# Kernel optimization log

Measured on AMD Instinct MI355X. Metric: run time of the kernel, lower is better.

The kernel has to match this reference:

```python
import jax, jax.numpy as jnp
import numpy as np

LN_EPS = 1e-5

def _ln(x):
    # haiku LayerNorm([-1], create_scale=False, create_offset=False)
    mu = x.mean(axis=-1, keepdims=True)
    var = x.var(axis=-1, keepdims=True)
    return (x - mu) * jax.lax.rsqrt(var + LN_EPS)

def setup_inputs() -> dict:
    key = jax.random.key(0)
    ks = jax.random.split(key, 10)
    N, L, P = 512, 256, 64
    inp = {
        "local": jax.random.normal(ks[0], (N, L), jnp.float32),
        "pair": jax.random.normal(ks[1], (N, N, P), jnp.float32),
        "mask": jax.random.randint(ks[2], (N,), 0, 2, jnp.int32),
        "W_pair_gate": jax.random.normal(ks[3], (P, 2 * P), jnp.float32) / np.sqrt(P),
        "W_pair_value": jax.random.normal(ks[4], (P, 2 * P), jnp.float32) / np.sqrt(P),
        "W_left_gate": jax.random.normal(ks[5], (L, 2 * P), jnp.float32) / np.sqrt(L),
        "W_left_value": jax.random.normal(ks[6], (L, 2 * P), jnp.float32) / np.sqrt(L),
        "W_right_gate": jax.random.normal(ks[7], (L, 2 * P), jnp.float32) / np.sqrt(L),
        "W_right_value": jax.random.normal(ks[8], (L, 2 * P), jnp.float32) / np.sqrt(L),
        "W_out": jax.random.normal(ks[9], (3 * P, P), jnp.float32) / np.sqrt(3 * P),
    }
    return inp

def reference(local, pair, mask, W_pair_gate, W_pair_value, W_left_gate,
              W_left_value, W_right_gate, W_right_value, W_out):
    maskb = mask.astype(bool)
    pair_mask = maskb[:, None] & maskb[None, :]                  # (N, N)
    l = _ln(local)                                               # (N, L)
    p = _ln(pair)                                                # (N, N, P)
    pair_gate = p @ W_pair_gate                                  # (N, N, 2P)
    pair_value = p @ W_pair_value                                # (N, N, 2P)
    # left: broadcast local over axis 0/1, gelu-gate, mask, reduce over j
    left_gate = jax.nn.gelu((l @ W_left_gate)[:, None] + pair_gate)
    left_value = (l @ W_left_value)[None, :] + pair_value
    left = jnp.where(pair_mask[..., None], left_gate * left_value, 0).sum(axis=1)  # (N, 2P)
    right_gate = jax.nn.gelu((l @ W_right_gate)[None, :] + pair_gate)
    right_value = (l @ W_right_value)[:, None] + pair_value
    right = jnp.where(pair_mask[..., None], right_gate * right_value, 0).sum(axis=0)  # (N, 2P)
    paired_pseudo_local = _ln(left[:, None] + right[None, :])    # (N, N, 2P)
    pair_hidden = jnp.concatenate((p, paired_pseudo_local), axis=-1)  # (N, N, 3P)
    return pair_hidden @ W_out                                   # (N, N, P)
```

## Files before the change

### kernel.cpp

```cpp
#include <hip/hip_runtime.h>
#include <math.h>

#define LN_EPS 1e-5f


typedef __bf16 bf16x8 __attribute__((ext_vector_type(8)));
typedef float f32x16 __attribute__((ext_vector_type(16)));

__device__ __forceinline__ float gelu_f(float x) {
    float x2 = x * x;
    float e = __builtin_amdgcn_exp2f(x * fmaf(0.10294423f, x2, 2.3022079f));
    float r = __builtin_amdgcn_rcpf(e + 1.0f);
    return fmaf(-x, r, x);
}

__global__ void kM(const int* __restrict__ mask, int* __restrict__ act) {
    const int t = threadIdx.x;
    const int lane = t & 63, w = t >> 6;
    __shared__ int wcnt_sh[8];
    int m = (mask[t] != 0);
    unsigned long long b = __ballot(m);
    if (lane == 0) wcnt_sh[w] = __popcll(b);
    __syncthreads();
    int base = 0;
    for (int u = 0; u < w; ++u) base += wcnt_sh[u];
    int pos = base + __popcll(b & ((1ull << lane) - 1ull));
    if (m) act[1 + pos] = t;
    if (t == 511) act[0] = base + __popcll(b);
}

__global__ __launch_bounds__(256) void kA(
    const float* __restrict__ loc,
    const float* __restrict__ Wlg, const float* __restrict__ Wlv,
    const float* __restrict__ Wrg, const float* __restrict__ Wrv,
    float* __restrict__ proj) {
    __shared__ float ln_sh[8][260];
    __shared__ float red_sh[128][9];
    const int t = threadIdx.x;
    const int i0 = blockIdx.x * 8;
    const int mat = blockIdx.y;
    const float* __restrict__ W = (mat == 0) ? Wlg : (mat == 1) ? Wlv
                                 : (mat == 2) ? Wrg : Wrv;
    {
        int row = t >> 5, l32 = t & 31;
        const float4* src = (const float4*)(loc + (i0 + row) * 256);
        float4 v0 = src[l32 * 2];
        float4 v1 = src[l32 * 2 + 1];
        float s = (v0.x + v0.y) + (v0.z + v0.w) + (v1.x + v1.y) + (v1.z + v1.w);
        float ss = v0.x * v0.x + v0.y * v0.y + v0.z * v0.z + v0.w * v0.w +
                   v1.x * v1.x + v1.y * v1.y + v1.z * v1.z + v1.w * v1.w;
#pragma unroll
        for (int off = 1; off < 32; off <<= 1) {
            s += __shfl_xor(s, off);
            ss += __shfl_xor(ss, off);
        }
        float mu = s * (1.f / 256.f);
        float rs = rsqrtf(ss * (1.f / 256.f) - mu * mu + LN_EPS);
        float4 o0, o1;
        o0.x = (v0.x - mu) * rs; o0.y = (v0.y - mu) * rs;
        o0.z = (v0.z - mu) * rs; o0.w = (v0.w - mu) * rs;
        o1.x = (v1.x - mu) * rs; o1.y = (v1.y - mu) * rs;
        o1.z = (v1.z - mu) * rs; o1.w = (v1.w - mu) * rs;
        *(float4*)&ln_sh[row][l32 * 8] = o0;
        *(float4*)&ln_sh[row][l32 * 8 + 4] = o1;
    }
    __syncthreads();

    const int n = t & 127;
    const int kh = t >> 7;
    float acc[8] = {0.f, 0.f, 0.f, 0.f, 0.f, 0.f, 0.f, 0.f};
#pragma unroll 2
    for (int c = 0; c < 32; ++c) {
        const int kc = kh * 128 + c * 4;
        float w0 = W[(kc + 0) * 128 + n];
        float w1 = W[(kc + 1) * 128 + n];
        float w2 = W[(kc + 2) * 128 + n];
        float w3 = W[(kc + 3) * 128 + n];
#pragma unroll
        for (int r = 0; r < 8; ++r) {
            float4 l4 = *(const float4*)&ln_sh[r][kc];
            acc[r] += l4.x * w0 + l4.y * w1 + l4.z * w2 + l4.w * w3;
        }
    }
    if (kh == 1) {
#pragma unroll
        for (int r = 0; r < 8; ++r) red_sh[n][r] = acc[r];
    }
    __syncthreads();
    if (kh == 0) {
#pragma unroll
        for (int r = 0; r < 8; ++r)
            proj[mat * 65536 + (i0 + r) * 128 + n] = acc[r] + red_sh[n][r];
    }
}

#define KB_TI 8
__global__ __launch_bounds__(256) void kB(
    const float* __restrict__ pair, const int* __restrict__ act,
    const float* __restrict__ Wg, const float* __restrict__ Wv,
    const float* __restrict__ lg, const float* __restrict__ lv,
    const float* __restrict__ rg, const float* __restrict__ rv,
    float* __restrict__ left, float* __restrict__ right) {
    __shared__ __bf16 A_sh[2][32][72];
    __shared__ float lv_sh[32][132];
    __shared__ float rg_sh[32][132];
    __shared__ int ji_sh[32];
    __shared__ int ii_sh[KB_TI];

    const int cnt = act[0];
    const int j0 = blockIdx.x * 32;
    const int ibase = blockIdx.y * KB_TI;
    if (j0 >= cnt || ibase >= cnt) return;
    const int nact = min(KB_TI, cnt - ibase);

    const int t = threadIdx.x;
    const int lane = t & 63;
    const int w = t >> 6;
    const int c = lane & 31;
    const int half = lane >> 5;
    const int n = w * 32 + c;

    if (t < 32) ji_sh[t] = act[1 + min(j0 + t, cnt - 1)];
    if (t >= 64 && t < 64 + KB_TI) ii_sh[t - 64] = act[1 + min(ibase + (t - 64), cnt - 1)];
    __syncthreads();

    bf16x8 bg[4], bv[4];
#pragma unroll
    for (int kt = 0; kt < 4; ++kt) {
        bf16x8 vg, vv;
#pragma unroll
        for (int e = 0; e < 8; ++e) {
            int kr = kt * 16 + half * 8 + e;
            vg[e] = (__bf16)Wg[kr * 128 + n];
            vv[e] = (__bf16)Wv[kr * 128 + n];
        }
        bg[kt] = vg; bv[kt] = vv;
    }

    for (int idx = t; idx < 32 * 128; idx += 256) {
        int jj = idx >> 7, nn = idx & 127;
        int j = ji_sh[jj];
        lv_sh[jj][nn] = lv[j * 128 + nn];
        rg_sh[jj][nn] = rg[j * 128 + nn];
    }

    const int srow = t >> 3;
    const int kseg = (t & 7) * 8;
    float4 p0, p1;
    float plg, prv;

    {
        int iF = act[1 + ibase];
        const float* src = pair + ((size_t)iF * 512 + ji_sh[srow]) * 64 + kseg;
        p0 = *(const float4*)src;
        p1 = *(const float4*)(src + 4);
        plg = lg[iF * 128 + n];
        prv = rv[iF * 128 + n];
    }

    auto lnwrite = [&](int buf) {
        float s = (p0.x + p0.y) + (p0.z + p0.w) + (p1.x + p1.y) + (p1.z + p1.w);
        float ss = p0.x * p0.x + p0.y * p0.y + p0.z * p0.z + p0.w * p0.w +
                   p1.x * p1.x + p1.y * p1.y + p1.z * p1.z + p1.w * p1.w;
        s += __shfl_xor(s, 1); ss += __shfl_xor(ss, 1);
        s += __shfl_xor(s, 2); ss += __shfl_xor(ss, 2);
        s += __shfl_xor(s, 4); ss += __shfl_xor(ss, 4);
        float mu = s * (1.f / 64.f);
        float rs = rsqrtf(ss * (1.f / 64.f) - mu * mu + LN_EPS);
        bf16x8 o;
        o[0] = (__bf16)((p0.x - mu) * rs); o[1] = (__bf16)((p0.y - mu) * rs);
        o[2] = (__bf16)((p0.z - mu) * rs); o[3] = (__bf16)((p0.w - mu) * rs);
        o[4] = (__bf16)((p1.x - mu) * rs); o[5] = (__bf16)((p1.y - mu) * rs);
        o[6] = (__bf16)((p1.z - mu) * rs); o[7] = (__bf16)((p1.w - mu) * rs);
        *(bf16x8*)&A_sh[buf][srow][kseg] = o;
    };
    lnwrite(0);
    __syncthreads();

    float racc[16];
#pragma unroll
    for (int r = 0; r < 16; ++r) racc[r] = 0.f;

    for (int ii = 0; ii < nact; ++ii) {
        const int i = ii_sh[ii];
        const float lgi = plg;
        const float rvi = prv;
        if (ii + 1 < nact) {
            int iF = ii_sh[ii + 1];
            const float* src = pair + ((size_t)iF * 512 + ji_sh[srow]) * 64 + kseg;
            p0 = *(const float4*)src;
            p1 = *(const float4*)(src + 4);
            plg = lg[iF * 128 + n];
            prv = rv[iF * 128 + n];
        }

        f32x16 ag = {}; f32x16 av = {};
#pragma unroll
        for (int kt = 0; kt < 4; ++kt) {
            bf16x8 af = *(const bf16x8*)&A_sh[ii & 1][c][kt * 16 + half * 8];
            ag = __builtin_amdgcn_mfma_f32_32x32x16_bf16(af, bg[kt], ag, 0, 0, 0);
            av = __builtin_amdgcn_mfma_f32_32x32x16_bf16(af, bv[kt], av, 0, 0, 0);
        }

        float lsum = 0.f;
#pragma unroll
        for (int r = 0; r < 16; ++r) {
            int m = 4 * half + (r & 3) + 8 * (r >> 2);
            float pg = ag[r], pv = av[r];
            float lres = gelu_f(lgi + pg) * (lv_sh[m][n] + pv);
            float rres = gelu_f(rg_sh[m][n] + pg) * (rvi + pv);
            if (j0 + m < cnt) lsum += lres;
            racc[r] += rres;
        }
        float tot = lsum + __shfl_xor(lsum, 32);
        if (lane < 32) atomicAdd(&left[i * 128 + n], tot);

        if (ii + 1 < nact) lnwrite((ii + 1) & 1);
        __syncthreads();
    }

#pragma unroll
    for (int r = 0; r < 16; ++r) {
        int m = 4 * half + (r & 3) + 8 * (r >> 2);
        if (j0 + m < cnt) atomicAdd(&right[ji_sh[m] * 128 + n], racc[r]);
    }
}

__global__ void kD1(const float* __restrict__ left, const float* __restrict__ right,
                    const float* __restrict__ W_out,
                    float* __restrict__ Aw, float* __restrict__ Bw,
                    float* __restrict__ sums, float* __restrict__ cs) {
    const int t = threadIdx.x;
    const int r = blockIdx.x;
    const int which = blockIdx.y;
    const float* src = which ? right : left;
    __shared__ float row_sh[128];
    __shared__ float red[4];
    float v = src[r * 128 + t];
    row_sh[t] = v;
    float s = v, ss = v * v;
#pragma unroll
    for (int off = 1; off < 64; off <<= 1) {
        s += __shfl_xor(s, off);
        ss += __shfl_xor(ss, off);
    }
    int wid = t >> 6, lane = t & 63;
    if (lane == 0) { red[wid * 2] = s; red[wid * 2 + 1] = ss; }
    __syncthreads();
    if (t == 0) {
        sums[which * 1024 + r] = red[0] + red[2];
        sums[which * 1024 + 512 + r] = red[1] + red[3];
    }
    if (t < 64) {
        float a = 0.f;
        const float* W2 = W_out + 64 * 64;
#pragma unroll 8
        for (int m = 0; m < 128; ++m) a += row_sh[m] * W2[m * 64 + t];
        (which ? Bw : Aw)[r * 64 + t] = a;
    }
    if (r == 0 && which == 0 && t < 64) {
        float c0 = 0.f, c1 = 0.f;
        for (int k = 0; k < 64; ++k) c0 += W_out[k * 64 + t];
        for (int m = 0; m < 128; ++m) c1 += W_out[(64 + m) * 64 + t];
        cs[t] = c0;
        cs[64 + t] = c1;
    }
}

__global__ void kD2(const float* __restrict__ left, const float* __restrict__ right,
                    float* __restrict__ C) {
    __shared__ float l_sh[32][68];
    __shared__ float r_sh[32][68];
    const int t = threadIdx.x;
    const int tx = t & 15, ty = t >> 4;
    const int i0 = blockIdx.x * 32, j0 = blockIdx.y * 32;
    float acc00 = 0.f, acc01 = 0.f, acc10 = 0.f, acc11 = 0.f;
    for (int kc = 0; kc < 128; kc += 64) {
        __syncthreads();
#pragma unroll
        for (int u = 0; u < 2; ++u) {
            int fi = t + u * 256;
            int row = fi >> 4, kq = (fi & 15) * 4;
            float4 lv4 = *(const float4*)(left + (i0 + row) * 128 + kc + kq);
            float4 rv4 = *(const float4*)(right + (j0 + row) * 128 + kc + kq);
            *(float4*)&l_sh[row][kq] = lv4;
            *(float4*)&r_sh[row][kq] = rv4;
        }
        __syncthreads();
#pragma unroll 8
        for (int k = 0; k < 64; ++k) {
            float l0 = l_sh[ty * 2 + 0][k], l1 = l_sh[ty * 2 + 1][k];
            float r0 = r_sh[tx * 2 + 0][k], r1 = r_sh[tx * 2 + 1][k];
            acc00 += l0 * r0; acc01 += l0 * r1;
            acc10 += l1 * r0; acc11 += l1 * r1;
        }
    }
    C[(size_t)(i0 + ty * 2 + 0) * 512 + j0 + tx * 2 + 0] = acc00;
    C[(size_t)(i0 + ty * 2 + 0) * 512 + j0 + tx * 2 + 1] = acc01;
    C[(size_t)(i0 + ty * 2 + 1) * 512 + j0 + tx * 2 + 0] = acc10;
    C[(size_t)(i0 + ty * 2 + 1) * 512 + j0 + tx * 2 + 1] = acc11;
}

__global__ __launch_bounds__(256) void kC(
    const float* __restrict__ pair, const float* __restrict__ Wout,
    const float* __restrict__ Aw, const float* __restrict__ Bw,
    const float* __restrict__ Cw, const float* __restrict__ sums,
    const float* __restrict__ cs, float* __restrict__ out) {
    __shared__ __bf16 A_sh[2][64][72];
    __shared__ float rs_sh[128], q_sh[128];

    const int t = threadIdx.x;
    const int lane = t & 63;
    const int w = t >> 6;
    const int c = lane & 31;
    const int half = lane >> 5;
    const int i0 = blockIdx.x * 2;
    const int j0 = blockIdx.y * 64;
    const int isub = w & 1;
    const int nt = w >> 1;
    const int n = nt * 32 + c;
    const int i = i0 + isub;

    bf16x8 bo[4];
#pragma unroll
    for (int kt = 0; kt < 4; ++kt) {
        bf16x8 v;
#pragma unroll
        for (int e = 0; e < 8; ++e)
            v[e] = (__bf16)Wout[(kt * 16 + half * 8 + e) * 64 + n];
        bo[kt] = v;
    }

    if (t < 128) {
        int ip = i0 + (t >> 6);
        int jp = j0 + (t & 63);
        float sumL = sums[ip], ssL = sums[512 + ip];
        float sR = sums[1024 + jp], ssR = sums[1536 + jp];
        float Cv = Cw[(size_t)ip * 512 + jp];
        float mu = (sumL + sR) * (1.f / 128.f);
        float var = (ssL + 2.f * Cv + ssR) * (1.f / 128.f) - mu * mu;
        float rs = rsqrtf(var + LN_EPS);
        rs_sh[t] = rs;
        q_sh[t] = rs * mu;
    }
    {
        int row = t >> 1;
        int kc = (t & 1) * 32;
        const float* src = pair + ((size_t)(i0 + (row >> 6)) * 512 + j0 + (row & 63)) * 64 + kc;
        float4 v[8];
#pragma unroll
        for (int u = 0; u < 8; ++u) v[u] = ((const float4*)src)[u];
        float s = 0.f, ss = 0.f;
#pragma unroll
        for (int u = 0; u < 8; ++u) {
            s += (v[u].x + v[u].y) + (v[u].z + v[u].w);
            ss += v[u].x * v[u].x + v[u].y * v[u].y + v[u].z * v[u].z + v[u].w * v[u].w;
        }
        s += __shfl_xor(s, 1); ss += __shfl_xor(ss, 1);
        float mu = s * (1.f / 64.f);
        float rs = rsqrtf(ss * (1.f / 64.f) - mu * mu + LN_EPS);
#pragma unroll
        for (int u = 0; u < 2; ++u) {
            bf16x8 o;
            o[0] = (__bf16)((v[u*2].x - mu) * rs);   o[1] = (__bf16)((v[u*2].y - mu) * rs);
            o[2] = (__bf16)((v[u*2].z - mu) * rs);   o[3] = (__bf16)((v[u*2].w - mu) * rs);
            o[4] = (__bf16)((v[u*2+1].x - mu) * rs); o[5] = (__bf16)((v[u*2+1].y - mu) * rs);
            o[6] = (__bf16)((v[u*2+1].z - mu) * rs); o[7] = (__bf16)((v[u*2+1].w - mu) * rs);
            *(bf16x8*)&A_sh[row >> 6][row & 63][kc + u * 8] = o;
        }
#pragma unroll
        for (int u = 2; u < 4; ++u) {
            bf16x8 o;
            o[0] = (__bf16)((v[u*2].x - mu) * rs);   o[1] = (__bf16)((v[u*2].y - mu) * rs);
            o[2] = (__bf16)((v[u*2].z - mu) * rs);   o[3] = (__bf16)((v[u*2].w - mu) * rs);
            o[4] = (__bf16)((v[u*2+1].x - mu) * rs); o[5] = (__bf16)((v[u*2+1].y - mu) * rs);
            o[6] = (__bf16)((v[u*2+1].z - mu) * rs); o[7] = (__bf16)((v[u*2+1].w - mu) * rs);
            *(bf16x8*)&A_sh[row >> 6][row & 63][kc + u * 8] = o;
        }
    }
    __syncthreads();

    f32x16 acc0 = {}; f32x16 acc1 = {};
#pragma unroll
    for (int kt = 0; kt < 4; ++kt) {
        bf16x8 a0 = *(const bf16x8*)&A_sh[isub][c][kt * 16 + half * 8];
        bf16x8 a1 = *(const bf16x8*)&A_sh[isub][32 + c][kt * 16 + half * 8];
        acc0 = __builtin_amdgcn_mfma_f32_32x32x16_bf16(a0, bo[kt], acc0, 0, 0, 0);
        acc1 = __builtin_amdgcn_mfma_f32_32x32x16_bf16(a1, bo[kt], acc1, 0, 0, 0);
    }

    const float A_in = Aw[i * 64 + n];
    const float cs1n = cs[64 + n];

#pragma unroll
    for (int mt = 0; mt < 2; ++mt) {
#pragma unroll
        for (int r = 0; r < 16; ++r) {
            int m = mt * 32 + 4 * half + (r & 3) + 8 * (r >> 2);
            float a = mt ? acc1[r] : acc0[r];
            float Bv = Bw[(j0 + m) * 64 + n];
            float rs = rs_sh[isub * 64 + m];
            float q = q_sh[isub * 64 + m];
            out[((size_t)i * 512 + j0 + m) * 64 + n] =
                fmaf(rs, A_in + Bv, fmaf(-q, cs1n, a));
        }
    }
}

extern "C" void kernel_launch(void* const* d_in, const int* in_sizes, int n_in,
                              void* d_out, int out_size, void* d_ws, size_t ws_size,
                              hipStream_t stream) {
    const float* loc  = (const float*)d_in[0];
    const float* pair = (const float*)d_in[1];
    const int*   mask = (const int*)d_in[2];
    const float* Wpg  = (const float*)d_in[3];
    const float* Wpv  = (const float*)d_in[4];
    const float* Wlg  = (const float*)d_in[5];
    const float* Wlv  = (const float*)d_in[6];
    const float* Wrg  = (const float*)d_in[7];
    const float* Wrv  = (const float*)d_in[8];
    const float* Wout = (const float*)d_in[9];
    float* out = (float*)d_out;
    float* ws = (float*)d_ws;

    float* proj  = ws;
    float* left  = ws + 262144;
    float* right = ws + 327680;
    float* Aw    = ws + 393216;
    float* Bw    = ws + 425984;
    float* Cw    = ws + 458752;
    float* sums  = ws + 720896;
    float* cs    = ws + 722944;
    int*   act   = (int*)(ws + 723072);

    hipMemsetAsync(left, 0, 2 * 65536 * sizeof(float), stream);

    kM<<<1, 512, 0, stream>>>(mask, act);
    kA<<<dim3(64, 4), 256, 0, stream>>>(loc, Wlg, Wlv, Wrg, Wrv, proj);
    kB<<<dim3(16, 64), 256, 0, stream>>>(pair, act, Wpg, Wpv,
                                         proj, proj + 65536, proj + 131072,
                                         proj + 196608, left, right);
    kD1<<<dim3(512, 2), 128, 0, stream>>>(left, right, Wout, Aw, Bw, sums, cs);
    kD2<<<dim3(16, 16), 256, 0, stream>>>(left, right, Cw);
    kC<<<dim3(256, 8), 256, 0, stream>>>(pair, Wout, Aw, Bw, Cw, sums, cs, out);
}
```

Baseline: 198.7 us.

## Fuse small kernels, drop memset, register-cache gathers, simplify output GEMM kernel

The mask compaction and the zeroing of the left/right buffers move into extra blocks of the projection kernel, which removes the memset and one launch. The two reduction kernels kD1/kD2 merge into one launch. kB keeps the gathered lv/rg values and a validity bitmask in registers instead of shared memory. kC now handles one row i per block and loads pair directly into MFMA operand registers, with no shared-memory staging and no barrier. It recomputes the per-(i,j) LayerNorm statistics inline in the epilogue, trading extra rsqrt work and repeated loads for fewer launches and less synchronisation.

```diff
diff --git a/kernel.cpp b/kernel.cpp
--- a/kernel.cpp
+++ b/kernel.cpp
@@ -14,29 +14,51 @@
     return fmaf(-x, r, x);
 }
 
-__global__ void kM(const int* __restrict__ mask, int* __restrict__ act) {
-    const int t = threadIdx.x;
-    const int lane = t & 63, w = t >> 6;
-    __shared__ int wcnt_sh[8];
-    int m = (mask[t] != 0);
-    unsigned long long b = __ballot(m);
-    if (lane == 0) wcnt_sh[w] = __popcll(b);
-    __syncthreads();
-    int base = 0;
-    for (int u = 0; u < w; ++u) base += wcnt_sh[u];
-    int pos = base + __popcll(b & ((1ull << lane) - 1ull));
-    if (m) act[1 + pos] = t;
-    if (t == 511) act[0] = base + __popcll(b);
-}
-
 __global__ __launch_bounds__(256) void kA(
     const float* __restrict__ loc,
     const float* __restrict__ Wlg, const float* __restrict__ Wlv,
     const float* __restrict__ Wrg, const float* __restrict__ Wrv,
-    float* __restrict__ proj) {
+    float* __restrict__ proj, const int* __restrict__ mask,
+    int* __restrict__ act, float* __restrict__ left, float* __restrict__ right) {
+    const int t = threadIdx.x;
+    if (blockIdx.x == 64) {
+        if (blockIdx.y == 1) {
+            float4 z = {0.f, 0.f, 0.f, 0.f};
+            for (int idx = t; idx < 16384; idx += 256) ((float4*)left)[idx] = z;
+        } else if (blockIdx.y == 2) {
+            float4 z = {0.f, 0.f, 0.f, 0.f};
+            for (int idx = t; idx < 16384; idx += 256) ((float4*)right)[idx] = z;
+        } else if (blockIdx.y == 0) {
+            __shared__ int cnt_sh[8];
+            const int lane = t & 63, wv = t >> 6;
+            int msave[2];
+            unsigned long long bsave[2];
+#pragma unroll
+            for (int ch = 0; ch < 2; ++ch) {
+                int m = (mask[ch * 256 + t] != 0);
+                unsigned long long b = __ballot(m);
+                if (lane == 0) cnt_sh[ch * 4 + wv] = __popcll(b);
+                msave[ch] = m;
+                bsave[ch] = b;
+            }
+            __syncthreads();
+#pragma unroll
+            for (int ch = 0; ch < 2; ++ch) {
+                int base = 0;
+                for (int u = 0; u < ch * 4 + wv; ++u) base += cnt_sh[u];
+                int pos = base + __popcll(bsave[ch] & ((1ull << lane) - 1ull));
+                if (msave[ch]) act[1 + pos] = ch * 256 + t;
+            }
+            if (t == 0) {
+                int ctot = 0;
+                for (int u = 0; u < 8; ++u) ctot += cnt_sh[u];
+                act[0] = ctot;
+            }
+        }
+        return;
+    }
     __shared__ float ln_sh[8][260];
     __shared__ float red_sh[128][9];
-    const int t = threadIdx.x;
     const int i0 = blockIdx.x * 8;
     const int mat = blockIdx.y;
     const float* __restrict__ W = (mat == 0) ? Wlg : (mat == 1) ? Wlv
@@ -102,8 +124,6 @@
     const float* __restrict__ rg, const float* __restrict__ rv,
     float* __restrict__ left, float* __restrict__ right) {
     __shared__ __bf16 A_sh[2][32][72];
-    __shared__ float lv_sh[32][132];
-    __shared__ float rg_sh[32][132];
     __shared__ int ji_sh[32];
     __shared__ int ii_sh[KB_TI];
 
@@ -137,20 +157,23 @@
         bg[kt] = vg; bv[kt] = vv;
     }
 
-    for (int idx = t; idx < 32 * 128; idx += 256) {
-        int jj = idx >> 7, nn = idx & 127;
-        int j = ji_sh[jj];
-        lv_sh[jj][nn] = lv[j * 128 + nn];
-        rg_sh[jj][nn] = rg[j * 128 + nn];
+    float lvr[16], rgr[16];
+    unsigned jmask = 0;
+#pragma unroll
+    for (int r = 0; r < 16; ++r) {
+        int m = 4 * half + (r & 3) + 8 * (r >> 2);
+        int j = ji_sh[m];
+        lvr[r] = lv[j * 128 + n];
+        rgr[r] = rg[j * 128 + n];
+        if (j0 + m < cnt) jmask |= (1u << r);
     }
 
     const int srow = t >> 3;
     const int kseg = (t & 7) * 8;
     float4 p0, p1;
     float plg, prv;
-
     {
-        int iF = act[1 + ibase];
+        int iF = ii_sh[0];
         const float* src = pair + ((size_t)iF * 512 + ji_sh[srow]) * 64 + kseg;
         p0 = *(const float4*)src;
         p1 = *(const float4*)(src + 4);
@@ -205,11 +228,10 @@
         float lsum = 0.f;
 #pragma unroll
         for (int r = 0; r < 16; ++r) {
-            int m = 4 * half + (r & 3) + 8 * (r >> 2);
             float pg = ag[r], pv = av[r];
-            float lres = gelu_f(lgi + pg) * (lv_sh[m][n] + pv);
-            float rres = gelu_f(rg_sh[m][n] + pg) * (rvi + pv);
-            if (j0 + m < cnt) lsum += lres;
+            float lres = gelu_f(lgi + pg) * (lvr[r] + pv);
+            float rres = gelu_f(rgr[r] + pg) * (rvi + pv);
+            lsum += ((jmask >> r) & 1) ? lres : 0.f;
             racc[r] += rres;
         }
         float tot = lsum + __shfl_xor(lsum, 32);
@@ -221,84 +243,89 @@
 
 #pragma unroll
     for (int r = 0; r < 16; ++r) {
-        int m = 4 * half + (r & 3) + 8 * (r >> 2);
-        if (j0 + m < cnt) atomicAdd(&right[ji_sh[m] * 128 + n], racc[r]);
-    }
-}
-
-__global__ void kD1(const float* __restrict__ left, const float* __restrict__ right,
-                    const float* __restrict__ W_out,
-                    float* __restrict__ Aw, float* __restrict__ Bw,
-                    float* __restrict__ sums, float* __restrict__ cs) {
+        if ((jmask >> r) & 1) {
+            int m = 4 * half + (r & 3) + 8 * (r >> 2);
+            atomicAdd(&right[ji_sh[m] * 128 + n], racc[r]);
+        }
+    }
+}
+
+__global__ __launch_bounds__(256) void kD(
+    const float* __restrict__ left, const float* __restrict__ right,
+    const float* __restrict__ W_out,
+    float* __restrict__ Aw, float* __restrict__ Bw,
+    float* __restrict__ sums, float* __restrict__ cs, float* __restrict__ C) {
+    const int bx = blockIdx.x;
     const int t = threadIdx.x;
-    const int r = blockIdx.x;
-    const int which = blockIdx.y;
-    const float* src = which ? right : left;
-    __shared__ float row_sh[128];
-    __shared__ float red[4];
-    float v = src[r * 128 + t];
-    row_sh[t] = v;
-    float s = v, ss = v * v;
-#pragma unroll
-    for (int off = 1; off < 64; off <<= 1) {
-        s += __shfl_xor(s, off);
-        ss += __shfl_xor(ss, off);
-    }
-    int wid = t >> 6, lane = t & 63;
-    if (lane == 0) { red[wid * 2] = s; red[wid * 2 + 1] = ss; }
-    __syncthreads();
-    if (t == 0) {
-        sums[which * 1024 + r] = red[0] + red[2];
-        sums[which * 1024 + 512 + r] = red[1] + red[3];
-    }
-    if (t < 64) {
-        float a = 0.f;
-        const float* W2 = W_out + 64 * 64;
+    if (bx < 256) {
+        __shared__ float l_sh[32][68];
+        __shared__ float r_sh[32][68];
+        const int tx = t & 15, ty = t >> 4;
+        const int i0 = (bx & 15) * 32, j0 = (bx >> 4) * 32;
+        float acc00 = 0.f, acc01 = 0.f, acc10 = 0.f, acc11 = 0.f;
+        for (int kc = 0; kc < 128; kc += 64) {
+            __syncthreads();
+#pragma unroll
+            for (int u = 0; u < 2; ++u) {
+                int fi = t + u * 256;
+                int row = fi >> 4, kq = (fi & 15) * 4;
+                float4 lv4 = *(const float4*)(left + (i0 + row) * 128 + kc + kq);
+                float4 rv4 = *(const float4*)(right + (j0 + row) * 128 + kc + kq);
+                *(float4*)&l_sh[row][kq] = lv4;
+                *(float4*)&r_sh[row][kq] = rv4;
+            }
+            __syncthreads();
 #pragma unroll 8
-        for (int m = 0; m < 128; ++m) a += row_sh[m] * W2[m * 64 + t];
-        (which ? Bw : Aw)[r * 64 + t] = a;
-    }
-    if (r == 0 && which == 0 && t < 64) {
-        float c0 = 0.f, c1 = 0.f;
-        for (int k = 0; k < 64; ++k) c0 += W_out[k * 64 + t];
-        for (int m = 0; m < 128; ++m) c1 += W_out[(64 + m) * 64 + t];
-        cs[t] = c0;
-        cs[64 + t] = c1;
-    }
-}
-
-__global__ void kD2(const float* __restrict__ left, const float* __restrict__ right,
-                    float* __restrict__ C) {
-    __shared__ float l_sh[32][68];
-    __shared__ float r_sh[32][68];
-    const int t = threadIdx.x;
-    const int tx = t & 15, ty = t >> 4;
-    const int i0 = blockIdx.x * 32, j0 = blockIdx.y * 32;
-    float acc00 = 0.f, acc01 = 0.f, acc10 = 0.f, acc11 = 0.f;
-    for (int kc = 0; kc < 128; kc += 64) {
+            for (int k = 0; k < 64; ++k) {
+                float l0 = l_sh[ty * 2 + 0][k], l1 = l_sh[ty * 2 + 1][k];
+                float r0 = r_sh[tx * 2 + 0][k], r1 = r_sh[tx * 2 + 1][k];
+                acc00 += l0 * r0; acc01 += l0 * r1;
+                acc10 += l1 * r0; acc11 += l1 * r1;
+            }
+        }
+        C[(size_t)(i0 + ty * 2 + 0) * 512 + j0 + tx * 2 + 0] = acc00;
+        C[(size_t)(i0 + ty * 2 + 0) * 512 + j0 + tx * 2 + 1] = acc01;
+        C[(size_t)(i0 + ty * 2 + 1) * 512 + j0 + tx * 2 + 0] = acc10;
+        C[(size_t)(i0 + ty * 2 + 1) * 512 + j0 + tx * 2 + 1] = acc11;
+    } else {
+        const int id = bx - 256;
+        const int which = id >> 8;
+        const int sub = t >> 7;
+        const int tt = t & 127;
+        const int r = (id & 255) * 2 + sub;
+        const float* src = which ? right : left;
+        __shared__ float row_sh[2][128];
+        __shared__ float red[2][4];
+        float v = src[r * 128 + tt];
+        row_sh[sub][tt] = v;
+        float s = v, ss = v * v;
+#pragma unroll
+        for (int off = 1; off < 64; off <<= 1) {
+            s += __shfl_xor(s, off);
+            ss += __shfl_xor(ss, off);
+        }
+        int wid = tt >> 6, lane = tt & 63;
+        if (lane == 0) { red[sub][wid * 2] = s; red[sub][wid * 2 + 1] = ss; }
         __syncthreads();
-#pragma unroll
-        for (int u = 0; u < 2; ++u) {
-            int fi = t + u * 256;
-            int row = fi >> 4, kq = (fi & 15) * 4;
-            float4 lv4 = *(const float4*)(left + (i0 + row) * 128 + kc + kq);
-            float4 rv4 = *(const float4*)(right + (j0 + row) * 128 + kc + kq);
-            *(float4*)&l_sh[row][kq] = lv4;
-            *(float4*)&r_sh[row][kq] = rv4;
-        }
-        __syncthreads();
+        if (tt == 0) {
+            sums[which * 1024 + r] = red[sub][0] + red[sub][2];
+            sums[which * 1024 + 512 + r] = red[sub][1] + red[sub][3];
+        }
+        if (tt < 64) {
+            float a = 0.f;
+            const float* W2 = W_out + 64 * 64;
 #pragma unroll 8
-        for (int k = 0; k < 64; ++k) {
-            float l0 = l_sh[ty * 2 + 0][k], l1 = l_sh[ty * 2 + 1][k];
-            float r0 = r_sh[tx * 2 + 0][k], r1 = r_sh[tx * 2 + 1][k];
-            acc00 += l0 * r0; acc01 += l0 * r1;
-            acc10 += l1 * r0; acc11 += l1 * r1;
-        }
-    }
-    C[(size_t)(i0 + ty * 2 + 0) * 512 + j0 + tx * 2 + 0] = acc00;
-    C[(size_t)(i0 + ty * 2 + 0) * 512 + j0 + tx * 2 + 1] = acc01;
-    C[(size_t)(i0 + ty * 2 + 1) * 512 + j0 + tx * 2 + 0] = acc10;
-    C[(size_t)(i0 + ty * 2 + 1) * 512 + j0 + tx * 2 + 1] = acc11;
+            for (int m = 0; m < 128; ++m) a += row_sh[sub][m] * W2[m * 64 + tt];
+            (which ? Bw : Aw)[r * 64 + tt] = a;
+        }
+        if (id == 0 && t < 64) {
+            float c0 = 0.f, c1 = 0.f;
+            for (int k = 0; k < 64; ++k) c0 += W_out[k * 64 + t];
+            for (int m = 0; m < 128; ++m) c1 += W_out[(64 + m) * 64 + t];
+            cs[t] = c0;
+            cs[64 + t] = c1;
+        }
+    }
 }
 
 __global__ __launch_bounds__(256) void kC(
@@ -306,104 +333,74 @@
     const float* __restrict__ Aw, const float* __restrict__ Bw,
     const float* __restrict__ Cw, const float* __restrict__ sums,
     const float* __restrict__ cs, float* __restrict__ out) {
-    __shared__ __bf16 A_sh[2][64][72];
-    __shared__ float rs_sh[128], q_sh[128];
-
     const int t = threadIdx.x;
     const int lane = t & 63;
     const int w = t >> 6;
     const int c = lane & 31;
     const int half = lane >> 5;
-    const int i0 = blockIdx.x * 2;
+    const int i = blockIdx.x;
     const int j0 = blockIdx.y * 64;
-    const int isub = w & 1;
+    const int mt = w & 1;
     const int nt = w >> 1;
     const int n = nt * 32 + c;
-    const int i = i0 + isub;
-
+    const int jrow = j0 + mt * 32 + c;
+
+    const float* __restrict__ asrc = pair + ((size_t)i * 512 + jrow) * 64 + half * 8;
+    float4 v[8];
+#pragma unroll
+    for (int kt = 0; kt < 4; ++kt) {
+        v[2 * kt] = *(const float4*)(asrc + kt * 16);
+        v[2 * kt + 1] = *(const float4*)(asrc + kt * 16 + 4);
+    }
     bf16x8 bo[4];
 #pragma unroll
     for (int kt = 0; kt < 4; ++kt) {
-        bf16x8 v;
+        bf16x8 bb;
 #pragma unroll
         for (int e = 0; e < 8; ++e)
-            v[e] = (__bf16)Wout[(kt * 16 + half * 8 + e) * 64 + n];
-        bo[kt] = v;
-    }
-
-    if (t < 128) {
-        int ip = i0 + (t >> 6);
-        int jp = j0 + (t & 63);
-        float sumL = sums[ip], ssL = sums[512 + ip];
-        float sR = sums[1024 + jp], ssR = sums[1536 + jp];
-        float Cv = Cw[(size_t)ip * 512 + jp];
-        float mu = (sumL + sR) * (1.f / 128.f);
-        float var = (ssL + 2.f * Cv + ssR) * (1.f / 128.f) - mu * mu;
-        float rs = rsqrtf(var + LN_EPS);
-        rs_sh[t] = rs;
-        q_sh[t] = rs * mu;
-    }
-    {
-        int row = t >> 1;
-        int kc = (t & 1) * 32;
-        const float* src = pair + ((size_t)(i0 + (row >> 6)) * 512 + j0 + (row & 63)) * 64 + kc;
-        float4 v[8];
-#pragma unroll
-        for (int u = 0; u < 8; ++u) v[u] = ((const float4*)src)[u];
-        float s = 0.f, ss = 0.f;
-#pragma unroll
-        for (int u = 0; u < 8; ++u) {
-            s += (v[u].x + v[u].y) + (v[u].z + v[u].w);
-            ss += v[u].x * v[u].x + v[u].y * v[u].y + v[u].z * v[u].z + v[u].w * v[u].w;
-        }
-        s += __shfl_xor(s, 1); ss += __shfl_xor(ss, 1);
-        float mu = s * (1.f / 64.f);
-        float rs = rsqrtf(ss * (1.f / 64.f) - mu * mu + LN_EPS);
+            bb[e] = (__bf16)Wout[(kt * 16 + half * 8 + e) * 64 + n];
+        bo[kt] = bb;
+    }
+    float s = 0.f, ss = 0.f;
+#pragma unroll
+    for (int u = 0; u < 8; ++u) {
+        s += (v[u].x + v[u].y) + (v[u].z + v[u].w);
+        ss += v[u].x * v[u].x + v[u].y * v[u].y + v[u].z * v[u].z + v[u].w * v[u].w;
+    }
+    s += __shfl_xor(s, 32);
+    ss += __shfl_xor(ss, 32);
+    float mu = s * (1.f / 64.f);
+    float rs = rsqrtf(ss * (1.f / 64.f) - mu * mu + LN_EPS);
+
+    f32x16 acc = {};
+#pragma unroll
+    for (int kt = 0; kt < 4; ++kt) {
+        bf16x8 af;
 #pragma unroll
         for (int u = 0; u < 2; ++u) {
-            bf16x8 o;
-            o[0] = (__bf16)((v[u*2].x - mu) * rs);   o[1] = (__bf16)((v[u*2].y - mu) * rs);
-            o[2] = (__bf16)((v[u*2].z - mu) * rs);   o[3] = (__bf16)((v[u*2].w - mu) * rs);
-            o[4] = (__bf16)((v[u*2+1].x - mu) * rs); o[5] = (__bf16)((v[u*2+1].y - mu) * rs);
-            o[6] = (__bf16)((v[u*2+1].z - mu) * rs); o[7] = (__bf16)((v[u*2+1].w - mu) * rs);
-            *(bf16x8*)&A_sh[row >> 6][row & 63][kc + u * 8] = o;
-        }
-#pragma unroll
-        for (int u = 2; u < 4; ++u) {
-            bf16x8 o;
-            o[0] = (__bf16)((v[u*2].x - mu) * rs);   o[1] = (__bf16)((v[u*2].y - mu) * rs);
-            o[2] = (__bf16)((v[u*2].z - mu) * rs);   o[3] = (__bf16)((v[u*2].w - mu) * rs);
-            o[4] = (__bf16)((v[u*2+1].x - mu) * rs); o[5] = (__bf16)((v[u*2+1].y - mu) * rs);
-            o[6] = (__bf16)((v[u*2+1].z - mu) * rs); o[7] = (__bf16)((v[u*2+1].w - mu) * rs);
-            *(bf16x8*)&A_sh[row >> 6][row & 63][kc + u * 8] = o;
-        }
-    }
-    __syncthreads();
-
-    f32x16 acc0 = {}; f32x16 acc1 = {};
-#pragma unroll
-    for (int kt = 0; kt < 4; ++kt) {
-        bf16x8 a0 = *(const bf16x8*)&A_sh[isub][c][kt * 16 + half * 8];
-        bf16x8 a1 = *(const bf16x8*)&A_sh[isub][32 + c][kt * 16 + half * 8];
-        acc0 = __builtin_amdgcn_mfma_f32_32x32x16_bf16(a0, bo[kt], acc0, 0, 0, 0);
-        acc1 = __builtin_amdgcn_mfma_f32_32x32x16_bf16(a1, bo[kt], acc1, 0, 0, 0);
+            float4 vv = v[2 * kt + u];
+            af[u * 4 + 0] = (__bf16)((vv.x - mu) * rs);
+            af[u * 4 + 1] = (__bf16)((vv.y - mu) * rs);
+            af[u * 4 + 2] = (__bf16)((vv.z - mu) * rs);
+            af[u * 4 + 3] = (__bf16)((vv.w - mu) * rs);
+        }
+        acc = __builtin_amdgcn_mfma_f32_32x32x16_bf16(af, bo[kt], acc, 0, 0, 0);
     }
 
     const float A_in = Aw[i * 64 + n];
     const float cs1n = cs[64 + n];
-
-#pragma unroll
-    for (int mt = 0; mt < 2; ++mt) {
-#pragma unroll
-        for (int r = 0; r < 16; ++r) {
-            int m = mt * 32 + 4 * half + (r & 3) + 8 * (r >> 2);
-            float a = mt ? acc1[r] : acc0[r];
-            float Bv = Bw[(j0 + m) * 64 + n];
-            float rs = rs_sh[isub * 64 + m];
-            float q = q_sh[isub * 64 + m];
-            out[((size_t)i * 512 + j0 + m) * 64 + n] =
-                fmaf(rs, A_in + Bv, fmaf(-q, cs1n, a));
-        }
+    const float sumLi = sums[i], ssLi = sums[512 + i];
+#pragma unroll
+    for (int r = 0; r < 16; ++r) {
+        int jp = j0 + mt * 32 + 4 * half + (r & 3) + 8 * (r >> 2);
+        float sR = sums[1024 + jp], ssR = sums[1536 + jp];
+        float Cv = Cw[(size_t)i * 512 + jp];
+        float Bv = Bw[jp * 64 + n];
+        float mu_s = (sumLi + sR) * (1.f / 128.f);
+        float var_s = fmaf(-mu_s, mu_s, (ssLi + 2.f * Cv + ssR) * (1.f / 128.f));
+        float rs_s = rsqrtf(var_s + LN_EPS);
+        out[((size_t)i * 512 + jp) * 64 + n] =
+            fmaf(rs_s, (A_in + Bv) - mu_s * cs1n, acc[r]);
     }
 }
 
@@ -433,14 +430,11 @@
     float* cs    = ws + 722944;
     int*   act   = (int*)(ws + 723072);
 
-    hipMemsetAsync(left, 0, 2 * 65536 * sizeof(float), stream);
-
-    kM<<<1, 512, 0, stream>>>(mask, act);
-    kA<<<dim3(64, 4), 256, 0, stream>>>(loc, Wlg, Wlv, Wrg, Wrv, proj);
+    kA<<<dim3(65, 4), 256, 0, stream>>>(loc, Wlg, Wlv, Wrg, Wrv, proj,
+                                        mask, act, left, right);
     kB<<<dim3(16, 64), 256, 0, stream>>>(pair, act, Wpg, Wpv,
                                          proj, proj + 65536, proj + 131072,
                                          proj + 196608, left, right);
-    kD1<<<dim3(512, 2), 128, 0, stream>>>(left, right, Wout, Aw, Bw, sums, cs);
-    kD2<<<dim3(16, 16), 256, 0, stream>>>(left, right, Cw);
-    kC<<<dim3(256, 8), 256, 0, stream>>>(pair, Wout, Aw, Bw, Cw, sums, cs, out);
-}
+    kD<<<768, 256, 0, stream>>>(left, right, Wout, Aw, Bw, sums, cs, Cw);
+    kC<<<dim3(512, 8), 256, 0, stream>>>(pair, Wout, Aw, Bw, Cw, sums, cs, out);
+}
```

Result: faster. 191.8 us (-3.5%).
